# Kernel optimization log

Measured on AMD Instinct MI355X. Metric: run time of the kernel, lower is better.

The kernel has to match this reference:

```python
import jax, jax.numpy as jnp
import numpy as np

N = 131072      # total nodes (1024 graphs x 128 feature-column nodes)
E = 2097152     # edges (avg degree 16)
G = 1024        # graphs in batch
H = 128         # hidden_dim


def setup_inputs() -> dict:
    key = jax.random.key(0)
    ks = jax.random.split(key, 16)
    s = 0.05
    inp = {
        "x": jax.random.normal(ks[0], (N, 1), dtype=jnp.float32),
        "edge_index": jax.random.randint(ks[1], (2, E), 0, N, dtype=jnp.int64),
        "edge_weight": jax.random.uniform(ks[2], (E,), dtype=jnp.float32),
        "batch": jnp.sort(jax.random.randint(ks[3], (N,), 0, G, dtype=jnp.int64)),
        # GCNConv weights (PyG convention: out = A_hat @ (x @ W) + b)
        "W1": jax.random.normal(ks[4], (1, H), dtype=jnp.float32) * s,
        "b1": jnp.zeros((H,), dtype=jnp.float32),
        "W2": jax.random.normal(ks[5], (H, 2 * H), dtype=jnp.float32) * s,
        "b2": jnp.zeros((2 * H,), dtype=jnp.float32),
        "W3": jax.random.normal(ks[6], (2 * H, H), dtype=jnp.float32) * s,
        "b3": jnp.zeros((H,), dtype=jnp.float32),
        # MLP head
        "Wf1": jax.random.normal(ks[7], (H, 32), dtype=jnp.float32) * s,
        "bf1": jnp.zeros((32,), dtype=jnp.float32),
        "Wf2": jax.random.normal(ks[8], (32, 2), dtype=jnp.float32) * s,
        "bf2": jnp.zeros((2,), dtype=jnp.float32),
    }
    return inp


def reference(x, edge_index, edge_weight, batch, W1, b1, W2, b2, W3, b3, Wf1, bf1, Wf2, bf2):
    # --- GCN normalization with self-loops (gcn_norm, symmetric) ---
    loops = jnp.arange(N, dtype=edge_index.dtype)
    row = jnp.concatenate([edge_index[0], loops])          # src
    col = jnp.concatenate([edge_index[1], loops])          # dst (aggregation target)
    w = jnp.concatenate([edge_weight, jnp.ones((N,), dtype=edge_weight.dtype)])
    deg = jax.ops.segment_sum(w, col, num_segments=N)
    dis = jnp.where(deg > 0, jax.lax.rsqrt(jnp.where(deg > 0, deg, 1.0)), 0.0)
    norm = dis[row] * w * dis[col]                         # [E+N]

    def gcn_conv(h, W, b):
        h = h @ W                                          # [N, out] dense transform
        msg = norm[:, None] * h[row]                       # gather + scale
        return jax.ops.segment_sum(msg, col, num_segments=N) + b

    h = jax.nn.relu(gcn_conv(x, W1, b1))
    h = jax.nn.relu(gcn_conv(h, W2, b2))
    h = jax.nn.relu(gcn_conv(h, W3, b3))

    # --- global_mean_pool over batch segment ids ---
    sums = jax.ops.segment_sum(h, batch, num_segments=G)   # [G, H]
    cnts = jax.ops.segment_sum(jnp.ones((N,), dtype=h.dtype), batch, num_segments=G)
    pooled = sums / jnp.maximum(cnts, 1.0)[:, None]

    # --- MLP head (dropout is identity at inference) ---
    z = jax.nn.relu(pooled @ Wf1 + bf1)
    logits = z @ Wf2 + bf2                                 # [G, 2]
    return logits
```

## Files before the change

kernel.cpp:

```cpp
#include <hip/hip_runtime.h>
#include <math.h>
#include <stdio.h>

#define NN 131072
#define EE 2097152
#define GG 1024
#define NSLICE 256
#define SLICE_SHIFT 9
#define SLICE_N 512
#define NCHUNK 256
#define CHUNK_E (EE / NCHUNK)
#define BCAP 96
#define PSPLIT 8

typedef _Float16 half_t;
typedef _Float16 f16x2 __attribute__((ext_vector_type(2)));
typedef _Float16 f16x4 __attribute__((ext_vector_type(4)));
typedef float f32x4 __attribute__((ext_vector_type(4)));


__global__ __launch_bounds__(256) void k_part(const int* __restrict__ ei,
                                              const float* __restrict__ w,
                                              int* __restrict__ cnts,
                                              uint2* __restrict__ ebuf) {
    __shared__ int cur[NSLICE];
    int t = threadIdx.x, c = blockIdx.x;
    cur[t] = 0;
    __syncthreads();
    int e0 = c * CHUNK_E;
    for (int e = e0 + t; e < e0 + CHUNK_E; e += 256) {
        int d = ei[EE + e];
        int r = ei[e];
        float ww = w[e];
        int b = d >> SLICE_SHIFT;
        int pos = atomicAdd(&cur[b], 1);
        if (pos < BCAP) {
            uint2 p;
            p.x = ((unsigned)(d & (SLICE_N - 1)) << 17) | (unsigned)r;
            p.y = __float_as_uint(ww);
            ebuf[((size_t)c * NSLICE + b) * BCAP + pos] = p;
        }
    }
    __syncthreads();
    cnts[c * NSLICE + t] = min(cur[t], BCAP);
}

__global__ __launch_bounds__(256) void k_stot(const int* __restrict__ cnts,
                                              int* __restrict__ sbase,
                                              int* __restrict__ offs) {
    __shared__ int part[NSLICE];
    int t = threadIdx.x;
    int sum = 0;
    for (int c = 0; c < NCHUNK; ++c) sum += cnts[c * NSLICE + t];
    part[t] = sum;
    __syncthreads();
    for (int off = 1; off < NSLICE; off <<= 1) {
        int v = (t >= off) ? part[t - off] : 0;
        __syncthreads();
        part[t] += v;
        __syncthreads();
    }
    sbase[t] = (t == 0) ? 0 : part[t - 1];
    if (t == NSLICE - 1) offs[NN] = part[NSLICE - 1];
}

__global__ __launch_bounds__(512) void k_slice(const int* __restrict__ cnts,
                                               const uint2* __restrict__ ebuf,
                                               const int* __restrict__ sbase,
                                               const float* __restrict__ x,
                                               int* __restrict__ offs,
                                               float2* __restrict__ xd,
                                               uint2* __restrict__ pairs) {
    __shared__ int hcur[SLICE_N];
    __shared__ float dg[SLICE_N];
    __shared__ int part[512];
    int t = threadIdx.x;
    int s = blockIdx.x;
    int wv = t >> 6, lane = t & 63;
    if (t < SLICE_N) { hcur[t] = 0; dg[t] = 1.0f; }
    __syncthreads();
    for (int c = wv; c < NCHUNK; c += 8) {
        int idx = c * NSLICE + s;
        int cnt = cnts[idx];
        const uint2* base = ebuf + (size_t)idx * BCAP;
        for (int i = lane; i < cnt; i += 64) {
            uint2 e = base[i];
            int dl = e.x >> 17;
            atomicAdd(&hcur[dl], 1);
            atomicAdd(&dg[dl], __uint_as_float(e.y));
        }
    }
    __syncthreads();
    int a = (t < SLICE_N) ? hcur[t] : 0;
    part[t] = a;
    __syncthreads();
    for (int off = 1; off < 512; off <<= 1) {
        int v = (t >= off) ? part[t - off] : 0;
        __syncthreads();
        part[t] += v;
        __syncthreads();
    }
    int ex = (t == 0) ? 0 : part[t - 1];
    int g0 = sbase[s] + ex;
    int nb = s * SLICE_N;
    if (t < SLICE_N) {
        hcur[t] = g0;
        offs[nb + t] = g0;
        float2 v0;
        v0.x = x[nb + t];
        v0.y = rsqrtf(dg[t]);
        xd[nb + t] = v0;
    }
    __syncthreads();
    for (int c = wv; c < NCHUNK; c += 8) {
        int idx = c * NSLICE + s;
        int cnt = cnts[idx];
        const uint2* base = ebuf + (size_t)idx * BCAP;
        for (int i = lane; i < cnt; i += 64) {
            uint2 e = base[i];
            int dl = e.x >> 17;
            int pos = atomicAdd(&hcur[dl], 1);
            uint2 p;
            p.x = e.x & 0x1FFFF;
            p.y = e.y;
            pairs[pos] = p;
        }
    }
}

__global__ __launch_bounds__(256) void k_norm_s(const float2* __restrict__ xd,
                                                const int* __restrict__ offs,
                                                uint2* __restrict__ pairs,
                                                float* __restrict__ sarr) {
    int n = (blockIdx.x * 256 + threadIdx.x) >> 6;
    int lane = threadIdx.x & 63;
    float2 xdn = xd[n];
    float dn = xdn.y;
    int k0 = offs[n], k1 = offs[n + 1];
    float s = 0.f;
    for (int kb = k0; kb < k1; kb += 64) {
        int k = kb + lane;
        if (k < k1) {
            uint2 p = pairs[k];
            float2 xr = xd[p.x];
            float nrm = dn * __uint_as_float(p.y) * xr.y;
            pairs[k].y = __float_as_uint(nrm);
            s = fmaf(nrm, xr.x, s);
        }
    }
#pragma unroll
    for (int off = 32; off > 0; off >>= 1) s += __shfl_xor(s, off);
    if (lane == 0) sarr[n] = fmaf(dn * dn, xdn.x, s);
}

__global__ __launch_bounds__(256) void k_prop0r(const float* __restrict__ sarr,
                                                const float2* __restrict__ xd,
                                                const int* __restrict__ offs,
                                                const uint2* __restrict__ pairs,
                                                const float* __restrict__ W1,
                                                const float* __restrict__ b1,
                                                half_t* __restrict__ Bout) {
    int n = (blockIdx.x * 256 + threadIdx.x) >> 6;
    int lane = threadIdx.x & 63;
    float2 wv = ((const float2*)W1)[lane];
    float2 bv = ((const float2*)b1)[lane];
    float dn = xd[n].y;
    float sn = dn * dn;
    float sown = sarr[n];
    float accx = sn * fmaxf(fmaf(sown, wv.x, bv.x), 0.f);
    float accy = sn * fmaxf(fmaf(sown, wv.y, bv.y), 0.f);
    float ax1 = 0.f, ay1 = 0.f, ax2 = 0.f, ay2 = 0.f, ax3 = 0.f, ay3 = 0.f;
    int k0 = offs[n], k1 = offs[n + 1];
    int k = k0;
    for (; k + 4 <= k1; k += 4) {
        uint2 p0 = pairs[k], p1 = pairs[k + 1], p2 = pairs[k + 2], p3 = pairs[k + 3];
        float s0 = sarr[p0.x], s1 = sarr[p1.x], s2 = sarr[p2.x], s3 = sarr[p3.x];
        float n0 = __uint_as_float(p0.y), n1 = __uint_as_float(p1.y);
        float n2 = __uint_as_float(p2.y), n3 = __uint_as_float(p3.y);
        accx = fmaf(n0, fmaxf(fmaf(s0, wv.x, bv.x), 0.f), accx);
        accy = fmaf(n0, fmaxf(fmaf(s0, wv.y, bv.y), 0.f), accy);
        ax1 = fmaf(n1, fmaxf(fmaf(s1, wv.x, bv.x), 0.f), ax1);
        ay1 = fmaf(n1, fmaxf(fmaf(s1, wv.y, bv.y), 0.f), ay1);
        ax2 = fmaf(n2, fmaxf(fmaf(s2, wv.x, bv.x), 0.f), ax2);
        ay2 = fmaf(n2, fmaxf(fmaf(s2, wv.y, bv.y), 0.f), ay2);
        ax3 = fmaf(n3, fmaxf(fmaf(s3, wv.x, bv.x), 0.f), ax3);
        ay3 = fmaf(n3, fmaxf(fmaf(s3, wv.y, bv.y), 0.f), ay3);
    }
    for (; k < k1; ++k) {
        uint2 p = pairs[k];
        float sv = sarr[p.x];
        float nm = __uint_as_float(p.y);
        accx = fmaf(nm, fmaxf(fmaf(sv, wv.x, bv.x), 0.f), accx);
        accy = fmaf(nm, fmaxf(fmaf(sv, wv.y, bv.y), 0.f), accy);
    }
    accx = (accx + ax1) + (ax2 + ax3);
    accy = (accy + ay1) + (ay2 + ay3);
    f16x2 o;
    o.x = (half_t)accx;
    o.y = (half_t)accy;
    ((f16x2*)Bout)[(size_t)n * 64 + lane] = o;
}

__global__ __launch_bounds__(256) void k_wp(const float* __restrict__ W2,
                                            const float* __restrict__ W3,
                                            half_t* __restrict__ W2p,
                                            half_t* __restrict__ W3p) {
    int t = blockIdx.x * 256 + threadIdx.x;
    if (t < 32768) {
        int slot = t & 3, lane = (t >> 2) & 63, ks = (t >> 8) & 7, nt = t >> 11;
        int col = nt * 16 + (lane & 15);
        int k = ks * 16 + (lane >> 4) * 4 + slot;
        W2p[t] = (half_t)W2[k * 256 + col];
    } else {
        int u = t - 32768;
        int slot = u & 3, lane = (u >> 2) & 63, ks = (u >> 8) & 15, nt = u >> 12;
        int col = nt * 16 + (lane & 15);
        int k = ks * 16 + (lane >> 4) * 4 + slot;
        W3p[u] = (half_t)W3[k * 128 + col];
    }
}

__global__ __launch_bounds__(256) void k_gemm23(const half_t* __restrict__ Bh,
                                                const half_t* __restrict__ W2p,
                                                const float* __restrict__ b2,
                                                const half_t* __restrict__ W3p,
                                                half_t* __restrict__ Ah) {
    __shared__ __align__(16) char CtB[128 * 512];
    int n0 = blockIdx.x * 128;
    int t = threadIdx.x;
    int wv = t >> 6;
    int lane = t & 63;
    int lr = lane & 15;
    int lc = lane >> 4;

    f16x4 aA[8], aB[8];
    {
        const char* rowA = (const char*)(Bh + (size_t)(n0 + wv * 32 + lr) * 128) + lc * 8;
        const char* rowB = rowA + 16 * 128 * 2;
#pragma unroll
        for (int ks = 0; ks < 8; ++ks) {
            aA[ks] = *(const f16x4*)(rowA + ks * 32);
            aB[ks] = *(const f16x4*)(rowB + ks * 32);
        }
    }
    const f16x4* w2f = (const f16x4*)W2p;
    f32x4 accA[16], accB[16];
#pragma unroll
    for (int nt = 0; nt < 16; ++nt) {
        accA[nt] = (f32x4){0.f, 0.f, 0.f, 0.f};
        accB[nt] = (f32x4){0.f, 0.f, 0.f, 0.f};
    }
#pragma unroll
    for (int ks = 0; ks < 8; ++ks) {
#pragma unroll
        for (int h = 0; h < 2; ++h) {
            f16x4 b[8];
#pragma unroll
            for (int j = 0; j < 8; ++j) b[j] = w2f[((h * 8 + j) * 8 + ks) * 64 + lane];
#pragma unroll
            for (int j = 0; j < 8; ++j) {
                accA[h * 8 + j] = __builtin_amdgcn_mfma_f32_16x16x16f16(aA[ks], b[j], accA[h * 8 + j], 0, 0, 0);
                accB[h * 8 + j] = __builtin_amdgcn_mfma_f32_16x16x16f16(aB[ks], b[j], accB[h * 8 + j], 0, 0, 0);
            }
        }
    }
#pragma unroll
    for (int nt = 0; nt < 16; ++nt) {
        float bias = b2[nt * 16 + lr];
        int coff = (nt * 16 + lr) * 2;
#pragma unroll
        for (int r = 0; r < 4; ++r) {
            int rowA_ = wv * 32 + lc * 4 + r;
            int rowB_ = rowA_ + 16;
            float vA = fmaxf(accA[nt][r] + bias, 0.f);
            float vB = fmaxf(accB[nt][r] + bias, 0.f);
            *(half_t*)(CtB + rowA_ * 512 + (coff ^ ((rowA_ & 7) << 4))) = (half_t)vA;
            *(half_t*)(CtB + rowB_ * 512 + (coff ^ ((rowB_ & 7) << 4))) = (half_t)vB;
        }
    }
    __syncthreads();

    f16x4 a3A[16], a3B[16];
    {
        int rowA_ = wv * 32 + lr;
        int rowB_ = rowA_ + 16;
        const char* baseA = CtB + rowA_ * 512;
        const char* baseB = CtB + rowB_ * 512;
        int swA = (rowA_ & 7) << 4;
        int swB = (rowB_ & 7) << 4;
#pragma unroll
        for (int ks = 0; ks < 16; ++ks) {
            a3A[ks] = *(const f16x4*)(baseA + ((ks * 32 + lc * 8) ^ swA));
            a3B[ks] = *(const f16x4*)(baseB + ((ks * 32 + lc * 8) ^ swB));
        }
    }
    const f16x4* w3f = (const f16x4*)W3p;
    f32x4 acc3A[8], acc3B[8];
#pragma unroll
    for (int nt = 0; nt < 8; ++nt) {
        acc3A[nt] = (f32x4){0.f, 0.f, 0.f, 0.f};
        acc3B[nt] = (f32x4){0.f, 0.f, 0.f, 0.f};
    }
#pragma unroll
    for (int ks = 0; ks < 16; ++ks) {
        f16x4 cfr[8];
#pragma unroll
        for (int nt = 0; nt < 8; ++nt) cfr[nt] = w3f[(nt * 16 + ks) * 64 + lane];
#pragma unroll
        for (int nt = 0; nt < 8; ++nt) {
            acc3A[nt] = __builtin_amdgcn_mfma_f32_16x16x16f16(a3A[ks], cfr[nt], acc3A[nt], 0, 0, 0);
            acc3B[nt] = __builtin_amdgcn_mfma_f32_16x16x16f16(a3B[ks], cfr[nt], acc3B[nt], 0, 0, 0);
        }
    }
#pragma unroll
    for (int nt = 0; nt < 8; ++nt) {
#pragma unroll
        for (int r = 0; r < 4; ++r) {
            int rowA_ = n0 + wv * 32 + lc * 4 + r;
            Ah[(size_t)rowA_ * 128 + nt * 16 + lr] = (half_t)acc3A[nt][r];
            Ah[(size_t)(rowA_ + 16) * 128 + nt * 16 + lr] = (half_t)acc3B[nt][r];
        }
    }
}

__global__ __launch_bounds__(256) void k_proppool(const half_t* __restrict__ Ain,
                                                  const float2* __restrict__ xd,
                                                  const int* __restrict__ offs,
                                                  const uint2* __restrict__ pairs,
                                                  const float* __restrict__ b3,
                                                  const int* __restrict__ batch,
                                                  float* __restrict__ ppart) {
    __shared__ float psum[4 * 128];
    int b = blockIdx.x;
    int g = b >> 3, q = b & 7;
    int t = threadIdx.x;
    int wv = t >> 6, lane = t & 63;
    for (int i = t; i < 512; i += 256) psum[i] = 0.f;
    __syncthreads();
    int lo = 0, hi = NN;
    while (lo < hi) { int mid = (lo + hi) >> 1; if (batch[mid] < g) lo = mid + 1; else hi = mid; }
    int s0 = lo;
    lo = s0; hi = NN;
    while (lo < hi) { int mid = (lo + hi) >> 1; if (batch[mid] < g + 1) lo = mid + 1; else hi = mid; }
    int s1 = lo;
    const f16x2* A2 = (const f16x2*)Ain;
    float2 bv = ((const float2*)b3)[lane];
    for (int n = s0 + q * 4 + wv; n < s1; n += 32) {
        float dn = xd[n].y;
        float sn = dn * dn;
        f16x2 av = A2[(size_t)n * 64 + lane];
        float ax0 = sn * (float)av.x, ay0 = sn * (float)av.y;
        float ax1 = 0.f, ay1 = 0.f, ax2 = 0.f, ay2 = 0.f, ax3 = 0.f, ay3 = 0.f;
        int k0 = offs[n], k1 = offs[n + 1];
        int k = k0;
        for (; k + 8 <= k1; k += 8) {
            uint2 p0 = pairs[k],     p1 = pairs[k + 1], p2 = pairs[k + 2], p3 = pairs[k + 3];
            uint2 p4 = pairs[k + 4], p5 = pairs[k + 5], p6 = pairs[k + 6], p7 = pairs[k + 7];
            f16x2 r0 = A2[(size_t)p0.x * 64 + lane];
            f16x2 r1 = A2[(size_t)p1.x * 64 + lane];
            f16x2 r2 = A2[(size_t)p2.x * 64 + lane];
            f16x2 r3 = A2[(size_t)p3.x * 64 + lane];
            f16x2 r4 = A2[(size_t)p4.x * 64 + lane];
            f16x2 r5 = A2[(size_t)p5.x * 64 + lane];
            f16x2 r6 = A2[(size_t)p6.x * 64 + lane];
            f16x2 r7 = A2[(size_t)p7.x * 64 + lane];
            ax0 = fmaf(__uint_as_float(p0.y), (float)r0.x, ax0);
            ay0 = fmaf(__uint_as_float(p0.y), (float)r0.y, ay0);
            ax1 = fmaf(__uint_as_float(p1.y), (float)r1.x, ax1);
            ay1 = fmaf(__uint_as_float(p1.y), (float)r1.y, ay1);
            ax2 = fmaf(__uint_as_float(p2.y), (float)r2.x, ax2);
            ay2 = fmaf(__uint_as_float(p2.y), (float)r2.y, ay2);
            ax3 = fmaf(__uint_as_float(p3.y), (float)r3.x, ax3);
            ay3 = fmaf(__uint_as_float(p3.y), (float)r3.y, ay3);
            ax0 = fmaf(__uint_as_float(p4.y), (float)r4.x, ax0);
            ay0 = fmaf(__uint_as_float(p4.y), (float)r4.y, ay0);
            ax1 = fmaf(__uint_as_float(p5.y), (float)r5.x, ax1);
            ay1 = fmaf(__uint_as_float(p5.y), (float)r5.y, ay1);
            ax2 = fmaf(__uint_as_float(p6.y), (float)r6.x, ax2);
            ay2 = fmaf(__uint_as_float(p6.y), (float)r6.y, ay2);
            ax3 = fmaf(__uint_as_float(p7.y), (float)r7.x, ax3);
            ay3 = fmaf(__uint_as_float(p7.y), (float)r7.y, ay3);
        }
        for (; k + 4 <= k1; k += 4) {
            uint2 p0 = pairs[k], p1 = pairs[k + 1], p2 = pairs[k + 2], p3 = pairs[k + 3];
            f16x2 r0 = A2[(size_t)p0.x * 64 + lane];
            f16x2 r1 = A2[(size_t)p1.x * 64 + lane];
            f16x2 r2 = A2[(size_t)p2.x * 64 + lane];
            f16x2 r3 = A2[(size_t)p3.x * 64 + lane];
            ax0 = fmaf(__uint_as_float(p0.y), (float)r0.x, ax0);
            ay0 = fmaf(__uint_as_float(p0.y), (float)r0.y, ay0);
            ax1 = fmaf(__uint_as_float(p1.y), (float)r1.x, ax1);
            ay1 = fmaf(__uint_as_float(p1.y), (float)r1.y, ay1);
            ax2 = fmaf(__uint_as_float(p2.y), (float)r2.x, ax2);
            ay2 = fmaf(__uint_as_float(p2.y), (float)r2.y, ay2);
            ax3 = fmaf(__uint_as_float(p3.y), (float)r3.x, ax3);
            ay3 = fmaf(__uint_as_float(p3.y), (float)r3.y, ay3);
        }
        for (; k < k1; ++k) {
            uint2 p = pairs[k];
            f16x2 rv = A2[(size_t)p.x * 64 + lane];
            ax0 = fmaf(__uint_as_float(p.y), (float)rv.x, ax0);
            ay0 = fmaf(__uint_as_float(p.y), (float)rv.y, ay0);
        }
        float accx = (ax0 + ax1) + (ax2 + ax3);
        float accy = (ay0 + ay1) + (ay2 + ay3);
        accx = fmaxf(accx + bv.x, 0.f);
        accy = fmaxf(accy + bv.y, 0.f);
        psum[wv * 128 + 2 * lane]     += accx;
        psum[wv * 128 + 2 * lane + 1] += accy;
    }
    __syncthreads();
    if (t < 128) {
        ppart[(size_t)b * 128 + t] = psum[t] + psum[128 + t] + psum[256 + t] + psum[384 + t];
    }
}

__global__ __launch_bounds__(128) void k_mlp(const float* __restrict__ ppart,
                                             const int* __restrict__ batch,
                                             const float* __restrict__ Wf1,
                                             const float* __restrict__ bf1,
                                             const float* __restrict__ Wf2,
                                             const float* __restrict__ bf2,
                                             float* __restrict__ out) {
    __shared__ float p[128];
    __shared__ float z[32];
    int g = blockIdx.x;
    int t = threadIdx.x;
    int lo = 0, hi = NN;
    while (lo < hi) { int mid = (lo + hi) >> 1; if (batch[mid] < g) lo = mid + 1; else hi = mid; }
    int s0 = lo;
    lo = s0; hi = NN;
    while (lo < hi) { int mid = (lo + hi) >> 1; if (batch[mid] < g + 1) lo = mid + 1; else hi = mid; }
    int s1 = lo;
    float sum = 0.f;
#pragma unroll
    for (int q = 0; q < PSPLIT; ++q) sum += ppart[(size_t)(g * PSPLIT + q) * 128 + t];
    float c = (float)(s1 - s0);
    if (c < 1.f) c = 1.f;
    p[t] = sum / c;
    __syncthreads();
    if (t < 32) {
        float a = bf1[t];
        for (int k = 0; k < 128; ++k) a = fmaf(p[k], Wf1[k * 32 + t], a);
        z[t] = fmaxf(a, 0.f);
    }
    __syncthreads();
    if (t < 2) {
        float a = bf2[t];
        for (int j = 0; j < 32; ++j) a = fmaf(z[j], Wf2[j * 2 + t], a);
        out[g * 2 + t] = a;
    }
}

extern "C" void kernel_launch(void* const* d_in, const int* in_sizes, int n_in,
                              void* d_out, int out_size, void* d_ws, size_t ws_size,
                              hipStream_t stream) {
    const float* x   = (const float*)d_in[0];
    const int*   ei  = (const int*)d_in[1];
    const float* w   = (const float*)d_in[2];
    const int*   bat = (const int*)d_in[3];
    const float* W1  = (const float*)d_in[4];
    const float* b1  = (const float*)d_in[5];
    const float* W2  = (const float*)d_in[6];
    const float* b2  = (const float*)d_in[7];
    const float* W3  = (const float*)d_in[8];
    const float* b3  = (const float*)d_in[9];
    const float* Wf1 = (const float*)d_in[10];
    const float* bf1 = (const float*)d_in[11];
    const float* Wf2 = (const float*)d_in[12];
    const float* bf2 = (const float*)d_in[13];
    float* out = (float*)d_out;

    char* ws = (char*)d_ws;
    size_t o = 0;
    auto alloc = [&](size_t bytes) {
        void* p = ws + o;
        o += (bytes + 255) & ~(size_t)255;
        return p;
    };
    int*    offs   = (int*)alloc((size_t)(NN + 1) * 4);
    int*    sbase  = (int*)alloc((size_t)NSLICE * 4);
    int*    cnts   = (int*)alloc((size_t)NCHUNK * NSLICE * 4);
    uint2*  ebuf   = (uint2*)alloc((size_t)NCHUNK * NSLICE * BCAP * 8);
    float2* xd     = (float2*)alloc((size_t)NN * 8);
    float*  sarr   = (float*)alloc((size_t)NN * 4);
    uint2*  pairs  = (uint2*)alloc((size_t)EE * 8);
    half_t* Ah     = (half_t*)alloc((size_t)NN * 128 * 2);
    half_t* Bh     = (half_t*)alloc((size_t)NN * 128 * 2);
    half_t* W2p    = (half_t*)alloc((size_t)256 * 128 * 2);
    half_t* W3p    = (half_t*)alloc((size_t)128 * 256 * 2);
    float*  ppart  = (float*)alloc((size_t)GG * PSPLIT * 128 * 4);

    if (o > ws_size) {
        fprintf(stderr, "[kernel_launch] ws_size=%zu < needed=%zu — aborting launch\n",
                ws_size, o);
        return;
    }

    k_part<<<NCHUNK, 256, 0, stream>>>(ei, w, cnts, ebuf);
    k_stot<<<1, 256, 0, stream>>>(cnts, sbase, offs);
    k_slice<<<NSLICE, 512, 0, stream>>>(cnts, ebuf, sbase, x, offs, xd, pairs);
    k_wp<<<256, 256, 0, stream>>>(W2, W3, W2p, W3p);
    k_norm_s<<<NN / 4, 256, 0, stream>>>(xd, offs, pairs, sarr);
    k_prop0r<<<NN / 4, 256, 0, stream>>>(sarr, xd, offs, pairs, W1, b1, Bh);
    k_gemm23<<<NN / 128, 256, 0, stream>>>(Bh, W2p, b2, W3p, Ah);
    k_proppool<<<GG * PSPLIT, 256, 0, stream>>>(Ah, xd, offs, pairs, b3, bat, ppart);
    k_mlp<<<GG, 128, 0, stream>>>(ppart, bat, Wf1, bf1, Wf2, bf2, out);
}
```

Baseline: 461.7 us.

## Recompute edge norms on the fly instead of writing them back into pairs

The normalization kernel now uses 16 lanes per node instead of a full 64-lane wavefront. It no longer writes the per-edge norm back into the pairs array; instead it stores each node's scalar s together with its inverse-sqrt degree in a float2 array. Both propagation kernels rebuild each edge norm from dn, the raw weight and the source node's degree factor, which adds one small gather per edge. The pooling kernel also moves from 8 to 4 splits per graph, is launched as two half-batches, and drops from 8-way to 4-way unrolling. The aim is to cut global write traffic and idle lanes, accepting a little extra gather and FMA work in the hot propagation loops.

```diff
diff --git a/kernel.cpp b/kernel.cpp
--- a/kernel.cpp
+++ b/kernel.cpp
@@ -11,7 +11,7 @@
 #define NCHUNK 256
 #define CHUNK_E (EE / NCHUNK)
 #define BCAP 96
-#define PSPLIT 8
+#define PSPLIT 4
 
 typedef _Float16 half_t;
 typedef _Float16 f16x2 __attribute__((ext_vector_type(2)));
@@ -128,33 +128,33 @@
     }
 }
 
-__global__ __launch_bounds__(256) void k_norm_s(const float2* __restrict__ xd,
-                                                const int* __restrict__ offs,
-                                                uint2* __restrict__ pairs,
-                                                float* __restrict__ sarr) {
-    int n = (blockIdx.x * 256 + threadIdx.x) >> 6;
-    int lane = threadIdx.x & 63;
+__global__ __launch_bounds__(256) void k_s16(const float2* __restrict__ xd,
+                                             const int* __restrict__ offs,
+                                             const uint2* __restrict__ pairs,
+                                             float2* __restrict__ sd) {
+    int tid = blockIdx.x * 256 + threadIdx.x;
+    int n = tid >> 4;
+    int sl = tid & 15;
     float2 xdn = xd[n];
     float dn = xdn.y;
     int k0 = offs[n], k1 = offs[n + 1];
     float s = 0.f;
-    for (int kb = k0; kb < k1; kb += 64) {
-        int k = kb + lane;
-        if (k < k1) {
-            uint2 p = pairs[k];
-            float2 xr = xd[p.x];
-            float nrm = dn * __uint_as_float(p.y) * xr.y;
-            pairs[k].y = __float_as_uint(nrm);
-            s = fmaf(nrm, xr.x, s);
-        }
-    }
-#pragma unroll
-    for (int off = 32; off > 0; off >>= 1) s += __shfl_xor(s, off);
-    if (lane == 0) sarr[n] = fmaf(dn * dn, xdn.x, s);
-}
-
-__global__ __launch_bounds__(256) void k_prop0r(const float* __restrict__ sarr,
-                                                const float2* __restrict__ xd,
+    for (int k = k0 + sl; k < k1; k += 16) {
+        uint2 p = pairs[k];
+        float2 xr = xd[p.x];
+        s = fmaf(dn * __uint_as_float(p.y) * xr.y, xr.x, s);
+    }
+#pragma unroll
+    for (int off = 8; off > 0; off >>= 1) s += __shfl_xor(s, off, 16);
+    if (sl == 0) {
+        float2 v;
+        v.x = fmaf(dn * dn, xdn.x, s);
+        v.y = dn;
+        sd[n] = v;
+    }
+}
+
+__global__ __launch_bounds__(256) void k_prop0r(const float2* __restrict__ sd,
                                                 const int* __restrict__ offs,
                                                 const uint2* __restrict__ pairs,
                                                 const float* __restrict__ W1,
@@ -164,34 +164,36 @@
     int lane = threadIdx.x & 63;
     float2 wv = ((const float2*)W1)[lane];
     float2 bv = ((const float2*)b1)[lane];
-    float dn = xd[n].y;
+    float2 sdn = sd[n];
+    float dn = sdn.y;
     float sn = dn * dn;
-    float sown = sarr[n];
-    float accx = sn * fmaxf(fmaf(sown, wv.x, bv.x), 0.f);
-    float accy = sn * fmaxf(fmaf(sown, wv.y, bv.y), 0.f);
+    float accx = sn * fmaxf(fmaf(sdn.x, wv.x, bv.x), 0.f);
+    float accy = sn * fmaxf(fmaf(sdn.x, wv.y, bv.y), 0.f);
     float ax1 = 0.f, ay1 = 0.f, ax2 = 0.f, ay2 = 0.f, ax3 = 0.f, ay3 = 0.f;
     int k0 = offs[n], k1 = offs[n + 1];
     int k = k0;
     for (; k + 4 <= k1; k += 4) {
         uint2 p0 = pairs[k], p1 = pairs[k + 1], p2 = pairs[k + 2], p3 = pairs[k + 3];
-        float s0 = sarr[p0.x], s1 = sarr[p1.x], s2 = sarr[p2.x], s3 = sarr[p3.x];
-        float n0 = __uint_as_float(p0.y), n1 = __uint_as_float(p1.y);
-        float n2 = __uint_as_float(p2.y), n3 = __uint_as_float(p3.y);
-        accx = fmaf(n0, fmaxf(fmaf(s0, wv.x, bv.x), 0.f), accx);
-        accy = fmaf(n0, fmaxf(fmaf(s0, wv.y, bv.y), 0.f), accy);
-        ax1 = fmaf(n1, fmaxf(fmaf(s1, wv.x, bv.x), 0.f), ax1);
-        ay1 = fmaf(n1, fmaxf(fmaf(s1, wv.y, bv.y), 0.f), ay1);
-        ax2 = fmaf(n2, fmaxf(fmaf(s2, wv.x, bv.x), 0.f), ax2);
-        ay2 = fmaf(n2, fmaxf(fmaf(s2, wv.y, bv.y), 0.f), ay2);
-        ax3 = fmaf(n3, fmaxf(fmaf(s3, wv.x, bv.x), 0.f), ax3);
-        ay3 = fmaf(n3, fmaxf(fmaf(s3, wv.y, bv.y), 0.f), ay3);
+        float2 v0 = sd[p0.x], v1 = sd[p1.x], v2 = sd[p2.x], v3 = sd[p3.x];
+        float n0 = dn * __uint_as_float(p0.y) * v0.y;
+        float n1 = dn * __uint_as_float(p1.y) * v1.y;
+        float n2 = dn * __uint_as_float(p2.y) * v2.y;
+        float n3 = dn * __uint_as_float(p3.y) * v3.y;
+        accx = fmaf(n0, fmaxf(fmaf(v0.x, wv.x, bv.x), 0.f), accx);
+        accy = fmaf(n0, fmaxf(fmaf(v0.x, wv.y, bv.y), 0.f), accy);
+        ax1 = fmaf(n1, fmaxf(fmaf(v1.x, wv.x, bv.x), 0.f), ax1);
+        ay1 = fmaf(n1, fmaxf(fmaf(v1.x, wv.y, bv.y), 0.f), ay1);
+        ax2 = fmaf(n2, fmaxf(fmaf(v2.x, wv.x, bv.x), 0.f), ax2);
+        ay2 = fmaf(n2, fmaxf(fmaf(v2.x, wv.y, bv.y), 0.f), ay2);
+        ax3 = fmaf(n3, fmaxf(fmaf(v3.x, wv.x, bv.x), 0.f), ax3);
+        ay3 = fmaf(n3, fmaxf(fmaf(v3.x, wv.y, bv.y), 0.f), ay3);
     }
     for (; k < k1; ++k) {
         uint2 p = pairs[k];
-        float sv = sarr[p.x];
-        float nm = __uint_as_float(p.y);
-        accx = fmaf(nm, fmaxf(fmaf(sv, wv.x, bv.x), 0.f), accx);
-        accy = fmaf(nm, fmaxf(fmaf(sv, wv.y, bv.y), 0.f), accy);
+        float2 v = sd[p.x];
+        float nm = dn * __uint_as_float(p.y) * v.y;
+        accx = fmaf(nm, fmaxf(fmaf(v.x, wv.x, bv.x), 0.f), accx);
+        accy = fmaf(nm, fmaxf(fmaf(v.x, wv.y, bv.y), 0.f), accy);
     }
     accx = (accx + ax1) + (ax2 + ax3);
     accy = (accy + ay1) + (ay2 + ay3);
@@ -324,15 +326,16 @@
 }
 
 __global__ __launch_bounds__(256) void k_proppool(const half_t* __restrict__ Ain,
-                                                  const float2* __restrict__ xd,
+                                                  const float2* __restrict__ sd,
                                                   const int* __restrict__ offs,
                                                   const uint2* __restrict__ pairs,
                                                   const float* __restrict__ b3,
                                                   const int* __restrict__ batch,
-                                                  float* __restrict__ ppart) {
+                                                  float* __restrict__ ppart,
+                                                  int g0base) {
     __shared__ float psum[4 * 128];
     int b = blockIdx.x;
-    int g = b >> 3, q = b & 7;
+    int g = g0base + (b >> 2), q = b & 3;
     int t = threadIdx.x;
     int wv = t >> 6, lane = t & 63;
     for (int i = t; i < 512; i += 256) psum[i] = 0.f;
@@ -345,62 +348,39 @@
     int s1 = lo;
     const f16x2* A2 = (const f16x2*)Ain;
     float2 bv = ((const float2*)b3)[lane];
-    for (int n = s0 + q * 4 + wv; n < s1; n += 32) {
-        float dn = xd[n].y;
+    for (int n = s0 + q * 4 + wv; n < s1; n += 16) {
+        float dn = sd[n].y;
         float sn = dn * dn;
         f16x2 av = A2[(size_t)n * 64 + lane];
         float ax0 = sn * (float)av.x, ay0 = sn * (float)av.y;
         float ax1 = 0.f, ay1 = 0.f, ax2 = 0.f, ay2 = 0.f, ax3 = 0.f, ay3 = 0.f;
         int k0 = offs[n], k1 = offs[n + 1];
         int k = k0;
-        for (; k + 8 <= k1; k += 8) {
-            uint2 p0 = pairs[k],     p1 = pairs[k + 1], p2 = pairs[k + 2], p3 = pairs[k + 3];
-            uint2 p4 = pairs[k + 4], p5 = pairs[k + 5], p6 = pairs[k + 6], p7 = pairs[k + 7];
+        for (; k + 4 <= k1; k += 4) {
+            uint2 p0 = pairs[k], p1 = pairs[k + 1], p2 = pairs[k + 2], p3 = pairs[k + 3];
+            float n0 = dn * __uint_as_float(p0.y) * sd[p0.x].y;
+            float n1 = dn * __uint_as_float(p1.y) * sd[p1.x].y;
+            float n2 = dn * __uint_as_float(p2.y) * sd[p2.x].y;
+            float n3 = dn * __uint_as_float(p3.y) * sd[p3.x].y;
             f16x2 r0 = A2[(size_t)p0.x * 64 + lane];
             f16x2 r1 = A2[(size_t)p1.x * 64 + lane];
             f16x2 r2 = A2[(size_t)p2.x * 64 + lane];
             f16x2 r3 = A2[(size_t)p3.x * 64 + lane];
-            f16x2 r4 = A2[(size_t)p4.x * 64 + lane];
-            f16x2 r5 = A2[(size_t)p5.x * 64 + lane];
-            f16x2 r6 = A2[(size_t)p6.x * 64 + lane];
-            f16x2 r7 = A2[(size_t)p7.x * 64 + lane];
-            ax0 = fmaf(__uint_as_float(p0.y), (float)r0.x, ax0);
-            ay0 = fmaf(__uint_as_float(p0.y), (float)r0.y, ay0);
-            ax1 = fmaf(__uint_as_float(p1.y), (float)r1.x, ax1);
-            ay1 = fmaf(__uint_as_float(p1.y), (float)r1.y, ay1);
-            ax2 = fmaf(__uint_as_float(p2.y), (float)r2.x, ax2);
-            ay2 = fmaf(__uint_as_float(p2.y), (float)r2.y, ay2);
-            ax3 = fmaf(__uint_as_float(p3.y), (float)r3.x, ax3);
-            ay3 = fmaf(__uint_as_float(p3.y), (float)r3.y, ay3);
-            ax0 = fmaf(__uint_as_float(p4.y), (float)r4.x, ax0);
-            ay0 = fmaf(__uint_as_float(p4.y), (float)r4.y, ay0);
-            ax1 = fmaf(__uint_as_float(p5.y), (float)r5.x, ax1);
-            ay1 = fmaf(__uint_as_float(p5.y), (float)r5.y, ay1);
-            ax2 = fmaf(__uint_as_float(p6.y), (float)r6.x, ax2);
-            ay2 = fmaf(__uint_as_float(p6.y), (float)r6.y, ay2);
-            ax3 = fmaf(__uint_as_float(p7.y), (float)r7.x, ax3);
-            ay3 = fmaf(__uint_as_float(p7.y), (float)r7.y, ay3);
-        }
-        for (; k + 4 <= k1; k += 4) {
-            uint2 p0 = pairs[k], p1 = pairs[k + 1], p2 = pairs[k + 2], p3 = pairs[k + 3];
-            f16x2 r0 = A2[(size_t)p0.x * 64 + lane];
-            f16x2 r1 = A2[(size_t)p1.x * 64 + lane];
-            f16x2 r2 = A2[(size_t)p2.x * 64 + lane];
-            f16x2 r3 = A2[(size_t)p3.x * 64 + lane];
-            ax0 = fmaf(__uint_as_float(p0.y), (float)r0.x, ax0);
-            ay0 = fmaf(__uint_as_float(p0.y), (float)r0.y, ay0);
-            ax1 = fmaf(__uint_as_float(p1.y), (float)r1.x, ax1);
-            ay1 = fmaf(__uint_as_float(p1.y), (float)r1.y, ay1);
-            ax2 = fmaf(__uint_as_float(p2.y), (float)r2.x, ax2);
-            ay2 = fmaf(__uint_as_float(p2.y), (float)r2.y, ay2);
-            ax3 = fmaf(__uint_as_float(p3.y), (float)r3.x, ax3);
-            ay3 = fmaf(__uint_as_float(p3.y), (float)r3.y, ay3);
+            ax0 = fmaf(n0, (float)r0.x, ax0);
+            ay0 = fmaf(n0, (float)r0.y, ay0);
+            ax1 = fmaf(n1, (float)r1.x, ax1);
+            ay1 = fmaf(n1, (float)r1.y, ay1);
+            ax2 = fmaf(n2, (float)r2.x, ax2);
+            ay2 = fmaf(n2, (float)r2.y, ay2);
+            ax3 = fmaf(n3, (float)r3.x, ax3);
+            ay3 = fmaf(n3, (float)r3.y, ay3);
         }
         for (; k < k1; ++k) {
             uint2 p = pairs[k];
+            float nm = dn * __uint_as_float(p.y) * sd[p.x].y;
             f16x2 rv = A2[(size_t)p.x * 64 + lane];
-            ax0 = fmaf(__uint_as_float(p.y), (float)rv.x, ax0);
-            ay0 = fmaf(__uint_as_float(p.y), (float)rv.y, ay0);
+            ax0 = fmaf(nm, (float)rv.x, ax0);
+            ay0 = fmaf(nm, (float)rv.y, ay0);
         }
         float accx = (ax0 + ax1) + (ax2 + ax3);
         float accy = (ay0 + ay1) + (ay2 + ay3);
@@ -411,7 +391,8 @@
     }
     __syncthreads();
     if (t < 128) {
-        ppart[(size_t)b * 128 + t] = psum[t] + psum[128 + t] + psum[256 + t] + psum[384 + t];
+        int bb = (g - 0) * PSPLIT + q;
+        ppart[(size_t)bb * 128 + t] = psum[t] + psum[128 + t] + psum[256 + t] + psum[384 + t];
     }
 }
 
@@ -483,7 +464,7 @@
     int*    cnts   = (int*)alloc((size_t)NCHUNK * NSLICE * 4);
     uint2*  ebuf   = (uint2*)alloc((size_t)NCHUNK * NSLICE * BCAP * 8);
     float2* xd     = (float2*)alloc((size_t)NN * 8);
-    float*  sarr   = (float*)alloc((size_t)NN * 4);
+    float2* sd     = (float2*)alloc((size_t)NN * 8);
     uint2*  pairs  = (uint2*)alloc((size_t)EE * 8);
     half_t* Ah     = (half_t*)alloc((size_t)NN * 128 * 2);
     half_t* Bh     = (half_t*)alloc((size_t)NN * 128 * 2);
@@ -501,9 +482,10 @@
     k_stot<<<1, 256, 0, stream>>>(cnts, sbase, offs);
     k_slice<<<NSLICE, 512, 0, stream>>>(cnts, ebuf, sbase, x, offs, xd, pairs);
     k_wp<<<256, 256, 0, stream>>>(W2, W3, W2p, W3p);
-    k_norm_s<<<NN / 4, 256, 0, stream>>>(xd, offs, pairs, sarr);
-    k_prop0r<<<NN / 4, 256, 0, stream>>>(sarr, xd, offs, pairs, W1, b1, Bh);
+    k_s16<<<NN / 16, 256, 0, stream>>>(xd, offs, pairs, sd);
+    k_prop0r<<<NN / 4, 256, 0, stream>>>(sd, offs, pairs, W1, b1, Bh);
     k_gemm23<<<NN / 128, 256, 0, stream>>>(Bh, W2p, b2, W3p, Ah);
-    k_proppool<<<GG * PSPLIT, 256, 0, stream>>>(Ah, xd, offs, pairs, b3, bat, ppart);
+    k_proppool<<<(GG / 2) * PSPLIT, 256, 0, stream>>>(Ah, sd, offs, pairs, b3, bat, ppart, 0);
+    k_proppool<<<(GG / 2) * PSPLIT, 256, 0, stream>>>(Ah, sd, offs, pairs, b3, bat, ppart, GG / 2);
     k_mlp<<<GG, 128, 0, stream>>>(ppart, bat, Wf1, bf1, Wf2, bf2, out);
 }
```

New measurement: 499.8 us. +8.2%, slower.

## Use 16-lane subgroups per node in norm and layer-1 propagation kernels

Applied to the files above, without the earlier changes.

The degree/norm kernel now uses 16 lanes per node instead of a full 64-lane wavefront, so the lanes are not mostly idle at the average degree of about 16. The layer-1 propagation kernel now handles four nodes per wavefront: edge norms and neighbour scalars are loaded cooperatively into LDS, and every lane then loops over each node's staged edges for its two feature columns. The pooling-propagation split is halved, giving fewer blocks per graph. Risks include the LDS staging relying on an lgkmcnt wait without a barrier across lanes, and serial per-edge loops bounded by the largest degree in each group.

```diff
diff --git a/kernel.cpp b/kernel.cpp
--- a/kernel.cpp
+++ b/kernel.cpp
@@ -11,7 +11,7 @@
 #define NCHUNK 256
 #define CHUNK_E (EE / NCHUNK)
 #define BCAP 96
-#define PSPLIT 8
+#define PSPLIT 4
 
 typedef _Float16 half_t;
 typedef _Float16 f16x2 __attribute__((ext_vector_type(2)));
@@ -128,29 +128,27 @@
     }
 }
 
-__global__ __launch_bounds__(256) void k_norm_s(const float2* __restrict__ xd,
-                                                const int* __restrict__ offs,
-                                                uint2* __restrict__ pairs,
-                                                float* __restrict__ sarr) {
-    int n = (blockIdx.x * 256 + threadIdx.x) >> 6;
-    int lane = threadIdx.x & 63;
+__global__ __launch_bounds__(256) void k_s16(const float2* __restrict__ xd,
+                                             const int* __restrict__ offs,
+                                             uint2* __restrict__ pairs,
+                                             float* __restrict__ sarr) {
+    int tid = blockIdx.x * 256 + threadIdx.x;
+    int n = tid >> 4;
+    int sl = tid & 15;
     float2 xdn = xd[n];
     float dn = xdn.y;
     int k0 = offs[n], k1 = offs[n + 1];
     float s = 0.f;
-    for (int kb = k0; kb < k1; kb += 64) {
-        int k = kb + lane;
-        if (k < k1) {
-            uint2 p = pairs[k];
-            float2 xr = xd[p.x];
-            float nrm = dn * __uint_as_float(p.y) * xr.y;
-            pairs[k].y = __float_as_uint(nrm);
-            s = fmaf(nrm, xr.x, s);
-        }
-    }
-#pragma unroll
-    for (int off = 32; off > 0; off >>= 1) s += __shfl_xor(s, off);
-    if (lane == 0) sarr[n] = fmaf(dn * dn, xdn.x, s);
+    for (int k = k0 + sl; k < k1; k += 16) {
+        uint2 p = pairs[k];
+        float2 xr = xd[p.x];
+        float nrm = dn * __uint_as_float(p.y) * xr.y;
+        pairs[k].y = __float_as_uint(nrm);
+        s = fmaf(nrm, xr.x, s);
+    }
+#pragma unroll
+    for (int off = 8; off > 0; off >>= 1) s += __shfl_xor(s, off, 16);
+    if (sl == 0) sarr[n] = fmaf(dn * dn, xdn.x, s);
 }
 
 __global__ __launch_bounds__(256) void k_prop0r(const float* __restrict__ sarr,
@@ -160,45 +158,66 @@
                                                 const float* __restrict__ W1,
                                                 const float* __restrict__ b1,
                                                 half_t* __restrict__ Bout) {
-    int n = (blockIdx.x * 256 + threadIdx.x) >> 6;
-    int lane = threadIdx.x & 63;
-    float2 wv = ((const float2*)W1)[lane];
-    float2 bv = ((const float2*)b1)[lane];
-    float dn = xd[n].y;
-    float sn = dn * dn;
-    float sown = sarr[n];
-    float accx = sn * fmaxf(fmaf(sown, wv.x, bv.x), 0.f);
-    float accy = sn * fmaxf(fmaf(sown, wv.y, bv.y), 0.f);
-    float ax1 = 0.f, ay1 = 0.f, ax2 = 0.f, ay2 = 0.f, ax3 = 0.f, ay3 = 0.f;
+    __shared__ float2 buf[4][4][64];
+    int t = threadIdx.x;
+    int wv = t >> 6, lane = t & 63;
+    int sl = lane & 15, ng = lane >> 4;
+    int nbase = (blockIdx.x * 4 + wv) * 4;
+    int n = nbase + ng;
     int k0 = offs[n], k1 = offs[n + 1];
-    int k = k0;
-    for (; k + 4 <= k1; k += 4) {
-        uint2 p0 = pairs[k], p1 = pairs[k + 1], p2 = pairs[k + 2], p3 = pairs[k + 3];
-        float s0 = sarr[p0.x], s1 = sarr[p1.x], s2 = sarr[p2.x], s3 = sarr[p3.x];
-        float n0 = __uint_as_float(p0.y), n1 = __uint_as_float(p1.y);
-        float n2 = __uint_as_float(p2.y), n3 = __uint_as_float(p3.y);
-        accx = fmaf(n0, fmaxf(fmaf(s0, wv.x, bv.x), 0.f), accx);
-        accy = fmaf(n0, fmaxf(fmaf(s0, wv.y, bv.y), 0.f), accy);
-        ax1 = fmaf(n1, fmaxf(fmaf(s1, wv.x, bv.x), 0.f), ax1);
-        ay1 = fmaf(n1, fmaxf(fmaf(s1, wv.y, bv.y), 0.f), ay1);
-        ax2 = fmaf(n2, fmaxf(fmaf(s2, wv.x, bv.x), 0.f), ax2);
-        ay2 = fmaf(n2, fmaxf(fmaf(s2, wv.y, bv.y), 0.f), ay2);
-        ax3 = fmaf(n3, fmaxf(fmaf(s3, wv.x, bv.x), 0.f), ax3);
-        ay3 = fmaf(n3, fmaxf(fmaf(s3, wv.y, bv.y), 0.f), ay3);
-    }
-    for (; k < k1; ++k) {
-        uint2 p = pairs[k];
-        float sv = sarr[p.x];
-        float nm = __uint_as_float(p.y);
-        accx = fmaf(nm, fmaxf(fmaf(sv, wv.x, bv.x), 0.f), accx);
-        accy = fmaf(nm, fmaxf(fmaf(sv, wv.y, bv.y), 0.f), accy);
-    }
-    accx = (accx + ax1) + (ax2 + ax3);
-    accy = (accy + ay1) + (ay2 + ay3);
-    f16x2 o;
-    o.x = (half_t)accx;
-    o.y = (half_t)accy;
-    ((f16x2*)Bout)[(size_t)n * 64 + lane] = o;
+    int deg = k1 - k0;
+    int md = deg;
+    md = max(md, __shfl_xor(md, 16));
+    md = max(md, __shfl_xor(md, 32));
+    int rounds = (md + 63) >> 6;
+    if (rounds < 1) rounds = 1;
+    float2 wvp = ((const float2*)W1)[lane];
+    float2 bvp = ((const float2*)b1)[lane];
+    float sg = sarr[n];
+    float dgp = xd[n].y;
+    float accx[4] = {0.f, 0.f, 0.f, 0.f};
+    float accy[4] = {0.f, 0.f, 0.f, 0.f};
+    for (int rd = 0; rd < rounds; ++rd) {
+        int kbase = k0 + rd * 64;
+        int cnt = k1 - kbase;
+        if (cnt > 64) cnt = 64;
+#pragma unroll
+        for (int i = 0; i < 4; ++i) {
+            int idx = i * 16 + sl;
+            if (idx < cnt) {
+                uint2 p = pairs[kbase + idx];
+                float2 v;
+                v.x = __uint_as_float(p.y);
+                v.y = sarr[p.x];
+                buf[wv][ng][idx] = v;
+            }
+        }
+        asm volatile("s_waitcnt lgkmcnt(0)" ::: "memory");
+#pragma unroll
+        for (int nn = 0; nn < 4; ++nn) {
+            int kk0 = __shfl(k0, nn * 16);
+            int kk1 = __shfl(k1, nn * 16);
+            int c = kk1 - (kk0 + rd * 64);
+            if (c > 64) c = 64;
+            for (int e = 0; e < c; ++e) {
+                float2 v = buf[wv][nn][e];
+                accx[nn] = fmaf(v.x, fmaxf(fmaf(v.y, wvp.x, bvp.x), 0.f), accx[nn]);
+                accy[nn] = fmaf(v.x, fmaxf(fmaf(v.y, wvp.y, bvp.y), 0.f), accy[nn]);
+            }
+        }
+    }
+#pragma unroll
+    for (int nn = 0; nn < 4; ++nn) {
+        float so = __shfl(sg, nn * 16);
+        float dd = __shfl(dgp, nn * 16);
+        float sn = dd * dd;
+        float ax = fmaf(sn, fmaxf(fmaf(so, wvp.x, bvp.x), 0.f), accx[nn]);
+        float ay = fmaf(sn, fmaxf(fmaf(so, wvp.y, bvp.y), 0.f), accy[nn]);
+        f16x2 o;
+        o.x = (half_t)ax;
+        o.y = (half_t)ay;
+        ((f16x2*)Bout)[(size_t)(nbase + nn) * 64 + lane] = o;
+    }
 }
 
 __global__ __launch_bounds__(256) void k_wp(const float* __restrict__ W2,
@@ -332,7 +351,7 @@
                                                   float* __restrict__ ppart) {
     __shared__ float psum[4 * 128];
     int b = blockIdx.x;
-    int g = b >> 3, q = b & 7;
+    int g = b >> 2, q = b & 3;
     int t = threadIdx.x;
     int wv = t >> 6, lane = t & 63;
     for (int i = t; i < 512; i += 256) psum[i] = 0.f;
@@ -345,7 +364,7 @@
     int s1 = lo;
     const f16x2* A2 = (const f16x2*)Ain;
     float2 bv = ((const float2*)b3)[lane];
-    for (int n = s0 + q * 4 + wv; n < s1; n += 32) {
+    for (int n = s0 + q * 4 + wv; n < s1; n += 16) {
         float dn = xd[n].y;
         float sn = dn * dn;
         f16x2 av = A2[(size_t)n * 64 + lane];
@@ -501,8 +520,8 @@
     k_stot<<<1, 256, 0, stream>>>(cnts, sbase, offs);
     k_slice<<<NSLICE, 512, 0, stream>>>(cnts, ebuf, sbase, x, offs, xd, pairs);
     k_wp<<<256, 256, 0, stream>>>(W2, W3, W2p, W3p);
-    k_norm_s<<<NN / 4, 256, 0, stream>>>(xd, offs, pairs, sarr);
-    k_prop0r<<<NN / 4, 256, 0, stream>>>(sarr, xd, offs, pairs, W1, b1, Bh);
+    k_s16<<<NN / 16, 256, 0, stream>>>(xd, offs, pairs, sarr);
+    k_prop0r<<<NN / 16, 256, 0, stream>>>(sarr, xd, offs, pairs, W1, b1, Bh);
     k_gemm23<<<NN / 128, 256, 0, stream>>>(Bh, W2p, b2, W3p, Ah);
     k_proppool<<<GG * PSPLIT, 256, 0, stream>>>(Ah, xd, offs, pairs, b3, bat, ppart);
     k_mlp<<<GG, 128, 0, stream>>>(ppart, bat, Wf1, bf1, Wf2, bf2, out);
```

After: 398.9 us. -13.6%, faster.
